# Kernel optimization log

Hardware: AMD Instinct MI355X
Metric: run time of the kernel (lower is better)

The kernel has to match this reference:

```python
import jax, jax.numpy as jnp
import numpy as np

B, N, C, E, H = 2, 20000, 64, 640000, 16

def setup_inputs() -> dict:
    key = jax.random.key(0)
    ks = jax.random.split(key, 9)
    Q = jax.random.normal(ks[0], (B, N, C), dtype=jnp.float32)
    K = jax.random.normal(ks[1], (B, N, C), dtype=jnp.float32)
    V = jax.random.normal(ks[2], (B, N, C), dtype=jnp.float32)
    src = jax.random.randint(ks[3], (E,), 0, N, dtype=jnp.int32)
    dst = jax.random.randint(ks[4], (E,), 0, N, dtype=jnp.int32)
    efeat = jax.random.uniform(ks[5], (E, 2), dtype=jnp.float32)  # [s_norm, d_norm] in [0,1]
    W1 = jax.random.normal(ks[6], (2, H), dtype=jnp.float32) * 0.5
    b1 = jnp.zeros((H,), dtype=jnp.float32)
    W2 = jax.random.normal(ks[7], (H, 1), dtype=jnp.float32) * 0.5
    b2 = jnp.zeros((1,), dtype=jnp.float32)
    return {"Q": Q, "K": K, "V": V, "efeat": efeat, "W1": W1, "b1": b1,
            "W2": W2, "b2": b2, "src": src, "dst": dst}

def reference(Q, K, V, efeat, W1, b1, W2, b2, src, dst):
    n = Q.shape[1]
    # per-edge bias: MLP(e_ij) -> (E,)
    bias = (jax.nn.relu(efeat @ W1 + b1) @ W2 + b2)[:, 0]
    # per-edge logits: Q_dst . K_src  -> (E, B)
    logits = jnp.einsum('bec,bec->eb', Q[:, dst, :], K[:, src, :]) + bias[:, None]
    # segment softmax over incoming edges of each dst node
    seg_max = jax.ops.segment_max(logits, dst, num_segments=n)          # (N, B)
    exp_l = jnp.exp(logits - seg_max[dst])                               # (E, B)
    denom = jax.ops.segment_sum(exp_l, dst, num_segments=n)[dst]         # (E, B)
    alpha = exp_l / denom                                                # (E, B)
    # weighted aggregation of parent values: (E,B,C) scattered to (N,B,C)
    msg = alpha[:, :, None] * jnp.transpose(V[:, src, :], (1, 0, 2))
    H_msg = jax.ops.segment_sum(msg, dst, num_segments=n)                # (N, B, C)
    return jnp.transpose(H_msg, (1, 0, 2))                               # (B, N, C)
```

## Files before the change

kernel.cpp:

```cpp
#include <hip/hip_runtime.h>
#include <hip/hip_fp16.h>
#include <math.h>


#define EB_B 2
#define EB_C 64
#define EB_H 16

typedef _Float16 h2v __attribute__((ext_vector_type(2)));

__device__ __forceinline__ unsigned f2h2(float a, float b) {
    __half2 h = __floats2half2_rn(a, b);
    return *reinterpret_cast<unsigned*>(&h);
}
__device__ __forceinline__ float2 h2f2(unsigned u) {
    __half2 h = *reinterpret_cast<__half2*>(&u);
    return __half22float2(h);
}
__device__ __forceinline__ h2v bch2(unsigned u) {
    h2v r;
    __builtin_memcpy(&r, &u, 4);
    return r;
}

template <int CTRL>
__device__ __forceinline__ float dpp_add(float x) {
    int y = __builtin_amdgcn_update_dpp(0, __float_as_int(x), CTRL, 0xf, 0xf, true);
    return x + __int_as_float(y);
}
__device__ __forceinline__ float row16_allsum(float x) {
    x = dpp_add<0xB1>(x);
    x = dpp_add<0x4E>(x);
    x = dpp_add<0x124>(x);
    x = dpp_add<0x128>(x);
    return x;
}

__device__ __forceinline__ void build_bp(int* bp, const int* __restrict__ bsum,
                                         int NB) {
    if (threadIdx.x < (unsigned)NB) bp[threadIdx.x + 1] = bsum[threadIdx.x];
    if (threadIdx.x == 0) bp[0] = 0;
    __syncthreads();
    if (threadIdx.x == 0) {
        for (int j = 1; j <= NB; ++j) bp[j] += bp[j - 1];
    }
    __syncthreads();
}

__global__ __launch_bounds__(256) void eb_pack(
    const float4* __restrict__ K4, const float4* __restrict__ V4,
    uint4* __restrict__ kv, int total,
    int* __restrict__ cnt, int N) {
    int i = blockIdx.x * blockDim.x + threadIdx.x;
    if (i < N) cnt[i] = 0;
    if (i >= total) return;
    float4 k = K4[i];
    float4 v = V4[i];
    uint4 o;
    o.x = f2h2(k.x, k.y); o.y = f2h2(k.z, k.w);
    o.z = f2h2(v.x, v.y); o.w = f2h2(v.z, v.w);
    kv[i] = o;
}

__global__ void eb_count(const int* __restrict__ dst,
                         int* __restrict__ cnt,
                         int* __restrict__ slot, int E) {
    int e = blockIdx.x * blockDim.x + threadIdx.x;
    if (e < E) slot[e] = atomicAdd(&cnt[dst[e]], 1);
}

__global__ __launch_bounds__(1024) void eb_scan1(const int* __restrict__ cnt,
                                                 int* __restrict__ offs_loc,
                                                 int* __restrict__ bsum, int N) {
    __shared__ int wsum[16];
    int tid = threadIdx.x;
    int wv = tid >> 6, ln = tid & 63;
    int i = blockIdx.x * 1024 + tid;
    int v = (i < N) ? cnt[i] : 0;
    int x = v;
#pragma unroll
    for (int off = 1; off < 64; off <<= 1) {
        int t = __shfl_up(x, off, 64);
        if (ln >= off) x += t;
    }
    if (ln == 63) wsum[wv] = x;
    __syncthreads();
    if (wv == 0 && ln < 16) {
        int y = wsum[ln];
#pragma unroll
        for (int off = 1; off < 16; off <<= 1) {
            int t = __shfl_up(y, off, 64);
            if (ln >= off) y += t;
        }
        wsum[ln] = y;
    }
    __syncthreads();
    int base = (wv > 0 ? wsum[wv - 1] : 0);
    if (i < N) offs_loc[i] = base + x - v;
    if (tid == 1023) bsum[blockIdx.x] = base + x;
}

__global__ __launch_bounds__(256) void eb_fill_kernel(
    const int* __restrict__ dst, const int* __restrict__ src,
    const int* __restrict__ slot, const int* __restrict__ offs_loc,
    const int* __restrict__ bsum,
    const float2* __restrict__ efeat2,
    const float* __restrict__ W1, const float* __restrict__ b1,
    const float* __restrict__ W2, const float* __restrict__ b2,
    int2* __restrict__ ep, int E, int NB) {
    __shared__ int bp[33];
    build_bp(bp, bsum, NB);
    int e = blockIdx.x * blockDim.x + threadIdx.x;
    if (e >= E) return;
    float2 ef = efeat2[e];
    float acc = b2[0];
#pragma unroll
    for (int h = 0; h < EB_H; ++h) {
        float a = fmaf(ef.x, W1[h], fmaf(ef.y, W1[EB_H + h], b1[h]));
        a = fmaxf(a, 0.0f);
        acc = fmaf(a, W2[h], acc);
    }
    int d = dst[e];
    int pos = offs_loc[d] + bp[d >> 10] + slot[e];
    ep[pos] = make_int2(src[e], __float_as_int(acc));
}

__global__ __launch_bounds__(256) void eb_attn_fp16(
    const float4* __restrict__ Q4, const uint4* __restrict__ kv,
    const int2* __restrict__ ep, const int* __restrict__ offs_loc,
    const int* __restrict__ bsum,
    float4* __restrict__ out4, int N, int E, int NB) {
    __shared__ int bp[33];
    build_bp(bp, bsum, NB);
    int wave = threadIdx.x >> 6;
    int lane = threadIdx.x & 63;
    int task = blockIdx.x * 4 + wave;
    if (task >= N * EB_B) return;
    int b = (task >= N) ? 1 : 0;
    int n = task - (b ? N : 0);
    int g = lane >> 4;
    int cl = lane & 15;
    const size_t brow = (size_t)N * 16;
    float4 qf = Q4[(size_t)b * brow + (size_t)n * 16 + cl];
    h2v q01; q01[0] = (_Float16)qf.x; q01[1] = (_Float16)qf.y;
    h2v q23; q23[0] = (_Float16)qf.z; q23[1] = (_Float16)qf.w;
    const uint4* kvb = kv + (size_t)b * brow;
    int start = offs_loc[n] + bp[n >> 10];
    int end = (n + 1 < N) ? (offs_loc[n + 1] + bp[(n + 1) >> 10]) : E;
    int nit = (end - start + 7) >> 3;

    int eP = start + g;
    int2 c0 = ep[eP < end ? eP : 0];
    int2 c1 = ep[eP + 4 < end ? eP + 4 : 0];
    uint4 u0 = kvb[(size_t)c0.x * 16 + cl];
    uint4 u1 = kvb[(size_t)c1.x * 16 + cl];
    int eN = start + 8 + g;
    int2 n0 = ep[eN < end ? eN : 0];
    int2 n1 = ep[eN + 4 < end ? eN + 4 : 0];

    float s = 0.0f;
    float ax = 0.0f, ay = 0.0f, az = 0.0f, aw = 0.0f;

    for (int it = 0; it < nit; ++it) {
        uint4 fu0 = kvb[(size_t)n0.x * 16 + cl];
        uint4 fu1 = kvb[(size_t)n1.x * 16 + cl];
        int e2 = start + (it + 2) * 8 + g;
        int2 nn0 = ep[e2 < end ? e2 : 0];
        int2 nn1 = ep[e2 + 4 < end ? e2 + 4 : 0];
        int e0 = start + it * 8 + g;
        int e1 = e0 + 4;
        bool v0 = e0 < end;
        bool v1 = e1 < end;
        float p0 = __builtin_amdgcn_fdot2(q01, bch2(u0.x),
                   __builtin_amdgcn_fdot2(q23, bch2(u0.y), 0.0f, false), false);
        float p1 = __builtin_amdgcn_fdot2(q01, bch2(u1.x),
                   __builtin_amdgcn_fdot2(q23, bch2(u1.y), 0.0f, false), false);
        p0 = row16_allsum(p0);
        p1 = row16_allsum(p1);
        float l0 = fminf(p0 + __int_as_float(c0.y), 80.0f);
        float l1 = fminf(p1 + __int_as_float(c1.y), 80.0f);
        float w0 = v0 ? __expf(l0) : 0.0f;
        float w1 = v1 ? __expf(l1) : 0.0f;
        float2 va0 = h2f2(u0.z), vb0 = h2f2(u0.w);
        float2 va1 = h2f2(u1.z), vb1 = h2f2(u1.w);
        s += w0 + w1;
        ax = fmaf(w0, va0.x, fmaf(w1, va1.x, ax));
        ay = fmaf(w0, va0.y, fmaf(w1, va1.y, ay));
        az = fmaf(w0, vb0.x, fmaf(w1, vb1.x, az));
        aw = fmaf(w0, vb0.y, fmaf(w1, vb1.y, aw));
        c0 = n0; c1 = n1; u0 = fu0; u1 = fu1; n0 = nn0; n1 = nn1;
    }

    s  += __shfl_xor(s, 16);  s  += __shfl_xor(s, 32);
    ax += __shfl_xor(ax, 16); ax += __shfl_xor(ax, 32);
    ay += __shfl_xor(ay, 16); ay += __shfl_xor(ay, 32);
    az += __shfl_xor(az, 16); az += __shfl_xor(az, 32);
    aw += __shfl_xor(aw, 16); aw += __shfl_xor(aw, 32);

    if (lane < 16) {
        float inv = (end > start) ? 1.0f / s : 0.0f;
        float4 o;
        o.x = ax * inv; o.y = ay * inv; o.z = az * inv; o.w = aw * inv;
        out4[(size_t)b * brow + (size_t)n * 16 + cl] = o;
    }
}

__global__ __launch_bounds__(256) void eb_attn_f32(
    const float4* __restrict__ Q4, const float4* __restrict__ K4,
    const float4* __restrict__ V4,
    const int2* __restrict__ ep, const int* __restrict__ offs_loc,
    const int* __restrict__ bsum,
    float4* __restrict__ out4, int N, int E, int NB) {
    __shared__ int bp[33];
    build_bp(bp, bsum, NB);
    int wave = threadIdx.x >> 6;
    int lane = threadIdx.x & 63;
    int task = blockIdx.x * 4 + wave;
    if (task >= N * EB_B) return;
    int b = (task >= N) ? 1 : 0;
    int n = task - (b ? N : 0);
    int g = lane >> 4;
    int cl = lane & 15;
    const size_t brow = (size_t)N * 16;
    float4 q = Q4[(size_t)b * brow + (size_t)n * 16 + cl];
    const float4* Kb = K4 + (size_t)b * brow;
    const float4* Vb = V4 + (size_t)b * brow;
    int start = offs_loc[n] + bp[n >> 10];
    int end = (n + 1 < N) ? (offs_loc[n + 1] + bp[(n + 1) >> 10]) : E;
    int nit = (end - start + 3) >> 2;
    float s = 0.0f;
    float ax = 0.0f, ay = 0.0f, az = 0.0f, aw = 0.0f;
    for (int it = 0; it < nit; ++it) {
        int ei = start + it * 4 + g;
        bool valid = ei < end;
        int2 md = ep[valid ? ei : 0];
        float4 k = Kb[(size_t)md.x * 16 + cl];
        float4 v = Vb[(size_t)md.x * 16 + cl];
        float p = fmaf(q.x, k.x, fmaf(q.y, k.y, fmaf(q.z, k.z, q.w * k.w)));
        p = row16_allsum(p);
        float l = fminf(p + __int_as_float(md.y), 80.0f);
        float w = valid ? __expf(l) : 0.0f;
        s += w;
        ax = fmaf(w, v.x, ax);
        ay = fmaf(w, v.y, ay);
        az = fmaf(w, v.z, az);
        aw = fmaf(w, v.w, aw);
    }
    s  += __shfl_xor(s, 16);  s  += __shfl_xor(s, 32);
    ax += __shfl_xor(ax, 16); ax += __shfl_xor(ax, 32);
    ay += __shfl_xor(ay, 16); ay += __shfl_xor(ay, 32);
    az += __shfl_xor(az, 16); az += __shfl_xor(az, 32);
    aw += __shfl_xor(aw, 16); aw += __shfl_xor(aw, 32);
    if (lane < 16) {
        float inv = (end > start) ? 1.0f / s : 0.0f;
        float4 o;
        o.x = ax * inv; o.y = ay * inv; o.z = az * inv; o.w = aw * inv;
        out4[(size_t)b * brow + (size_t)n * 16 + cl] = o;
    }
}

extern "C" void kernel_launch(void* const* d_in, const int* in_sizes, int n_in,
                              void* d_out, int out_size, void* d_ws, size_t ws_size,
                              hipStream_t stream) {
    const float4* Q4  = (const float4*)d_in[0];
    const float4* K4  = (const float4*)d_in[1];
    const float4* V4  = (const float4*)d_in[2];
    const float2* ef2 = (const float2*)d_in[3];
    const float* W1   = (const float*)d_in[4];
    const float* b1   = (const float*)d_in[5];
    const float* W2   = (const float*)d_in[6];
    const float* b2   = (const float*)d_in[7];
    const int*   src  = (const int*)d_in[8];
    const int*   dst  = (const int*)d_in[9];
    float4* out4 = (float4*)d_out;

    const int E = in_sizes[8];
    const int N = in_sizes[0] / (EB_B * EB_C);
    const int total = EB_B * N * 16;

    char* base = (char*)d_ws;
    size_t off = 0;
    auto take = [&](size_t nbytes) {
        char* p = base + off;
        off += (nbytes + 15) & ~(size_t)15;
        return p;
    };
    int* offs_loc = (int*)take((size_t)N * 4);
    int* cnt      = (int*)take((size_t)N * 4);
    int* bsum     = (int*)take(64 * 4);
    int* slot     = (int*)take((size_t)E * 4);
    int2* ep      = (int2*)take((size_t)E * 8);
    uint4* kv     = (uint4*)take((size_t)total * 16);
    bool use_fp16 = off <= ws_size;

    const int tpb = 256;
    const int NB = (N + 1023) >> 10;
    eb_pack<<<(total + tpb - 1) / tpb, tpb, 0, stream>>>(
        K4, V4, kv, use_fp16 ? total : 0, cnt, N);
    eb_count<<<(E + tpb - 1) / tpb, tpb, 0, stream>>>(dst, cnt, slot, E);
    eb_scan1<<<NB, 1024, 0, stream>>>(cnt, offs_loc, bsum, N);
    eb_fill_kernel<<<(E + tpb - 1) / tpb, tpb, 0, stream>>>(
        dst, src, slot, offs_loc, bsum, ef2, W1, b1, W2, b2, ep, E, NB);

    int tasks = N * EB_B;
    int blks = (tasks + 3) / 4;
    if (use_fp16) {
        eb_attn_fp16<<<blks, tpb, 0, stream>>>(
            Q4, kv, ep, offs_loc, bsum, out4, N, E, NB);
    } else {
        eb_attn_f32<<<blks, tpb, 0, stream>>>(
            Q4, K4, V4, ep, offs_loc, bsum, out4, N, E, NB);
    }
}
```

Baseline: 92.40 us.

## Process both batches per wave in fp16 attention to share edge-list reads

Each wave now handles one destination node for both batch elements instead of one (node, batch) task. The CSR edge entries (src index and bias), the offsets and the loop control are loaded once and reused for both batches, and twice as many independent K/V gathers are in flight per iteration. This halves the grid size and raises register pressure from the duplicated accumulators and prefetch buffers, which may lower occupancy.

```diff
diff --git a/kernel.cpp b/kernel.cpp
--- a/kernel.cpp
+++ b/kernel.cpp
@@ -134,17 +134,19 @@
     build_bp(bp, bsum, NB);
     int wave = threadIdx.x >> 6;
     int lane = threadIdx.x & 63;
-    int task = blockIdx.x * 4 + wave;
-    if (task >= N * EB_B) return;
-    int b = (task >= N) ? 1 : 0;
-    int n = task - (b ? N : 0);
+    int n = blockIdx.x * 4 + wave;
+    if (n >= N) return;
     int g = lane >> 4;
     int cl = lane & 15;
     const size_t brow = (size_t)N * 16;
-    float4 qf = Q4[(size_t)b * brow + (size_t)n * 16 + cl];
-    h2v q01; q01[0] = (_Float16)qf.x; q01[1] = (_Float16)qf.y;
-    h2v q23; q23[0] = (_Float16)qf.z; q23[1] = (_Float16)qf.w;
-    const uint4* kvb = kv + (size_t)b * brow;
+    float4 qfa = Q4[(size_t)n * 16 + cl];
+    float4 qfb = Q4[brow + (size_t)n * 16 + cl];
+    h2v qa01; qa01[0] = (_Float16)qfa.x; qa01[1] = (_Float16)qfa.y;
+    h2v qa23; qa23[0] = (_Float16)qfa.z; qa23[1] = (_Float16)qfa.w;
+    h2v qb01; qb01[0] = (_Float16)qfb.x; qb01[1] = (_Float16)qfb.y;
+    h2v qb23; qb23[0] = (_Float16)qfb.z; qb23[1] = (_Float16)qfb.w;
+    const uint4* kv0 = kv;
+    const uint4* kv1 = kv + brow;
     int start = offs_loc[n] + bp[n >> 10];
     int end = (n + 1 < N) ? (offs_loc[n + 1] + bp[(n + 1) >> 10]) : E;
     int nit = (end - start + 7) >> 3;
@@ -152,18 +154,22 @@
     int eP = start + g;
     int2 c0 = ep[eP < end ? eP : 0];
     int2 c1 = ep[eP + 4 < end ? eP + 4 : 0];
-    uint4 u0 = kvb[(size_t)c0.x * 16 + cl];
-    uint4 u1 = kvb[(size_t)c1.x * 16 + cl];
+    uint4 u0a = kv0[(size_t)c0.x * 16 + cl];
+    uint4 u1a = kv0[(size_t)c1.x * 16 + cl];
+    uint4 u0b = kv1[(size_t)c0.x * 16 + cl];
+    uint4 u1b = kv1[(size_t)c1.x * 16 + cl];
     int eN = start + 8 + g;
     int2 n0 = ep[eN < end ? eN : 0];
     int2 n1 = ep[eN + 4 < end ? eN + 4 : 0];
 
-    float s = 0.0f;
-    float ax = 0.0f, ay = 0.0f, az = 0.0f, aw = 0.0f;
+    float sa = 0.0f, axa = 0.0f, aya = 0.0f, aza = 0.0f, awa = 0.0f;
+    float sb = 0.0f, axb = 0.0f, ayb = 0.0f, azb = 0.0f, awb = 0.0f;
 
     for (int it = 0; it < nit; ++it) {
-        uint4 fu0 = kvb[(size_t)n0.x * 16 + cl];
-        uint4 fu1 = kvb[(size_t)n1.x * 16 + cl];
+        uint4 fu0a = kv0[(size_t)n0.x * 16 + cl];
+        uint4 fu1a = kv0[(size_t)n1.x * 16 + cl];
+        uint4 fu0b = kv1[(size_t)n0.x * 16 + cl];
+        uint4 fu1b = kv1[(size_t)n1.x * 16 + cl];
         int e2 = start + (it + 2) * 8 + g;
         int2 nn0 = ep[e2 < end ? e2 : 0];
         int2 nn1 = ep[e2 + 4 < end ? e2 + 4 : 0];
@@ -171,37 +177,63 @@
         int e1 = e0 + 4;
         bool v0 = e0 < end;
         bool v1 = e1 < end;
-        float p0 = __builtin_amdgcn_fdot2(q01, bch2(u0.x),
-                   __builtin_amdgcn_fdot2(q23, bch2(u0.y), 0.0f, false), false);
-        float p1 = __builtin_amdgcn_fdot2(q01, bch2(u1.x),
-                   __builtin_amdgcn_fdot2(q23, bch2(u1.y), 0.0f, false), false);
-        p0 = row16_allsum(p0);
-        p1 = row16_allsum(p1);
-        float l0 = fminf(p0 + __int_as_float(c0.y), 80.0f);
-        float l1 = fminf(p1 + __int_as_float(c1.y), 80.0f);
-        float w0 = v0 ? __expf(l0) : 0.0f;
-        float w1 = v1 ? __expf(l1) : 0.0f;
-        float2 va0 = h2f2(u0.z), vb0 = h2f2(u0.w);
-        float2 va1 = h2f2(u1.z), vb1 = h2f2(u1.w);
-        s += w0 + w1;
-        ax = fmaf(w0, va0.x, fmaf(w1, va1.x, ax));
-        ay = fmaf(w0, va0.y, fmaf(w1, va1.y, ay));
-        az = fmaf(w0, vb0.x, fmaf(w1, vb1.x, az));
-        aw = fmaf(w0, vb0.y, fmaf(w1, vb1.y, aw));
-        c0 = n0; c1 = n1; u0 = fu0; u1 = fu1; n0 = nn0; n1 = nn1;
-    }
-
-    s  += __shfl_xor(s, 16);  s  += __shfl_xor(s, 32);
-    ax += __shfl_xor(ax, 16); ax += __shfl_xor(ax, 32);
-    ay += __shfl_xor(ay, 16); ay += __shfl_xor(ay, 32);
-    az += __shfl_xor(az, 16); az += __shfl_xor(az, 32);
-    aw += __shfl_xor(aw, 16); aw += __shfl_xor(aw, 32);
+        float p0a = __builtin_amdgcn_fdot2(qa01, bch2(u0a.x),
+                    __builtin_amdgcn_fdot2(qa23, bch2(u0a.y), 0.0f, false), false);
+        float p1a = __builtin_amdgcn_fdot2(qa01, bch2(u1a.x),
+                    __builtin_amdgcn_fdot2(qa23, bch2(u1a.y), 0.0f, false), false);
+        float p0b = __builtin_amdgcn_fdot2(qb01, bch2(u0b.x),
+                    __builtin_amdgcn_fdot2(qb23, bch2(u0b.y), 0.0f, false), false);
+        float p1b = __builtin_amdgcn_fdot2(qb01, bch2(u1b.x),
+                    __builtin_amdgcn_fdot2(qb23, bch2(u1b.y), 0.0f, false), false);
+        p0a = row16_allsum(p0a);
+        p1a = row16_allsum(p1a);
+        p0b = row16_allsum(p0b);
+        p1b = row16_allsum(p1b);
+        float b0 = __int_as_float(c0.y);
+        float b1_ = __int_as_float(c1.y);
+        float w0a = v0 ? __expf(fminf(p0a + b0, 80.0f)) : 0.0f;
+        float w1a = v1 ? __expf(fminf(p1a + b1_, 80.0f)) : 0.0f;
+        float w0b = v0 ? __expf(fminf(p0b + b0, 80.0f)) : 0.0f;
+        float w1b = v1 ? __expf(fminf(p1b + b1_, 80.0f)) : 0.0f;
+        float2 va0a = h2f2(u0a.z), vb0a = h2f2(u0a.w);
+        float2 va1a = h2f2(u1a.z), vb1a = h2f2(u1a.w);
+        float2 va0b = h2f2(u0b.z), vb0b = h2f2(u0b.w);
+        float2 va1b = h2f2(u1b.z), vb1b = h2f2(u1b.w);
+        sa += w0a + w1a;
+        axa = fmaf(w0a, va0a.x, fmaf(w1a, va1a.x, axa));
+        aya = fmaf(w0a, va0a.y, fmaf(w1a, va1a.y, aya));
+        aza = fmaf(w0a, vb0a.x, fmaf(w1a, vb1a.x, aza));
+        awa = fmaf(w0a, vb0a.y, fmaf(w1a, vb1a.y, awa));
+        sb += w0b + w1b;
+        axb = fmaf(w0b, va0b.x, fmaf(w1b, va1b.x, axb));
+        ayb = fmaf(w0b, va0b.y, fmaf(w1b, va1b.y, ayb));
+        azb = fmaf(w0b, vb0b.x, fmaf(w1b, vb1b.x, azb));
+        awb = fmaf(w0b, vb0b.y, fmaf(w1b, vb1b.y, awb));
+        c0 = n0; c1 = n1;
+        u0a = fu0a; u1a = fu1a; u0b = fu0b; u1b = fu1b;
+        n0 = nn0; n1 = nn1;
+    }
+
+    sa  += __shfl_xor(sa, 16);  sa  += __shfl_xor(sa, 32);
+    axa += __shfl_xor(axa, 16); axa += __shfl_xor(axa, 32);
+    aya += __shfl_xor(aya, 16); aya += __shfl_xor(aya, 32);
+    aza += __shfl_xor(aza, 16); aza += __shfl_xor(aza, 32);
+    awa += __shfl_xor(awa, 16); awa += __shfl_xor(awa, 32);
+    sb  += __shfl_xor(sb, 16);  sb  += __shfl_xor(sb, 32);
+    axb += __shfl_xor(axb, 16); axb += __shfl_xor(axb, 32);
+    ayb += __shfl_xor(ayb, 16); ayb += __shfl_xor(ayb, 32);
+    azb += __shfl_xor(azb, 16); azb += __shfl_xor(azb, 32);
+    awb += __shfl_xor(awb, 16); awb += __shfl_xor(awb, 32);
 
     if (lane < 16) {
-        float inv = (end > start) ? 1.0f / s : 0.0f;
-        float4 o;
-        o.x = ax * inv; o.y = ay * inv; o.z = az * inv; o.w = aw * inv;
-        out4[(size_t)b * brow + (size_t)n * 16 + cl] = o;
+        bool has = end > start;
+        float inva = has ? 1.0f / sa : 0.0f;
+        float invb = has ? 1.0f / sb : 0.0f;
+        float4 oa, ob;
+        oa.x = axa * inva; oa.y = aya * inva; oa.z = aza * inva; oa.w = awa * inva;
+        ob.x = axb * invb; ob.y = ayb * invb; ob.z = azb * invb; ob.w = awb * invb;
+        out4[(size_t)n * 16 + cl] = oa;
+        out4[brow + (size_t)n * 16 + cl] = ob;
     }
 }
 
@@ -302,13 +334,12 @@
     eb_fill_kernel<<<(E + tpb - 1) / tpb, tpb, 0, stream>>>(
         dst, src, slot, offs_loc, bsum, ef2, W1, b1, W2, b2, ep, E, NB);
 
-    int tasks = N * EB_B;
-    int blks = (tasks + 3) / 4;
     if (use_fp16) {
-        eb_attn_fp16<<<blks, tpb, 0, stream>>>(
+        eb_attn_fp16<<<(N + 3) / 4, tpb, 0, stream>>>(
             Q4, kv, ep, offs_loc, bsum, out4, N, E, NB);
     } else {
-        eb_attn_f32<<<blks, tpb, 0, stream>>>(
+        int tasks = N * EB_B;
+        eb_attn_f32<<<(tasks + 3) / 4, tpb, 0, stream>>>(
             Q4, K4, V4, ep, offs_loc, bsum, out4, N, E, NB);
     }
 }
```

After: 95.03 us. 2.8% more time.
